# Kernel tuning notes

Measured on AMD Instinct MI355X. Metric: run time of the kernel, lower is better.

## Reference

```python
import jax, jax.numpy as jnp
import numpy as np

EPS = 1e-5

def _conv(x, w, pad):
    # x: [B,C,H,W] NCHW, w: [O,I,kh,kw] OIHW
    return jax.lax.conv_general_dilated(
        x, w, (1, 1), [(pad, pad), (pad, pad)],
        dimension_numbers=('NCHW', 'OIHW', 'NCHW'))

def _bn(x, g, b, m, v):
    # eval-mode batchnorm folded into scale/shift
    s = g * jax.lax.rsqrt(v + EPS)
    return x * s[None, :, None, None] + (b - m * s)[None, :, None, None]

def _cbr(x, w, g, b, m, v):
    # Convolution block from CornerNet: conv3x3(pad=1, no bias) + BN + ReLU
    return jax.nn.relu(_bn(_conv(x, w, 1), g, b, m, v))


def setup_inputs() -> dict:
    key = jax.random.key(0)
    B, Cin, C, H, W = 4, 256, 256, 128, 128
    kdims = {'up': (C, Cin, 3, 3), 'down': (C, Cin, 3, 3),
             'p': (C, C, 3, 3), 'c1': (C, Cin, 1, 1), 'c2': (C, C, 3, 3)}
    inp = {'x': jax.random.normal(key, (B, Cin, H, W), dtype=jnp.float32)}
    for i, n in enumerate(['up', 'down', 'p', 'c1', 'c2']):
        ks = jax.random.split(jax.random.fold_in(key, i + 1), 5)
        inp['w_' + n] = jax.random.normal(ks[0], kdims[n], dtype=jnp.float32) * 0.02
        inp['g_' + n] = 1.0 + 0.1 * jax.random.normal(ks[1], (C,), dtype=jnp.float32)
        inp['b_' + n] = 0.1 * jax.random.normal(ks[2], (C,), dtype=jnp.float32)
        inp['m_' + n] = 0.1 * jax.random.normal(ks[3], (C,), dtype=jnp.float32)
        inp['v_' + n] = 0.5 + jax.random.uniform(ks[4], (C,), dtype=jnp.float32)
    return inp


def reference(x,
              w_up, g_up, b_up, m_up, v_up,
              w_down, g_down, b_down, m_down, v_down,
              w_p, g_p, b_p, m_p, v_p,
              w_c1, g_c1, b_c1, m_c1, v_c1,
              w_c2, g_c2, b_c2, m_c2, v_c2):
    # up branch: conv-bn-relu then LeftPool (reverse cummax over W) then RightPool (cummax over W)
    up = _cbr(x, w_up, g_up, b_up, m_up, v_up)
    up = jax.lax.cummax(up, axis=3, reverse=True)   # LeftPool
    up = jax.lax.cummax(up, axis=3)                 # RightPool
    # down branch: conv-bn-relu then TopPool (reverse cummax over H) then BottomPool (cummax over H)
    down = _cbr(x, w_down, g_down, b_down, m_down, v_down)
    down = jax.lax.cummax(down, axis=2, reverse=True)  # TopPool
    down = jax.lax.cummax(down, axis=2)                # BottomPool
    # merge path: 3x3 conv + BN on pooled sum
    merge = _bn(_conv(up + down, w_p, 1), g_p, b_p, m_p, v_p)
    # shortcut path: 1x1 conv + BN on input
    bn1 = _bn(_conv(x, w_c1, 0), g_c1, b_c1, m_c1, v_c1)
    relu1 = jax.nn.relu(merge + bn1)
    # output Convolution block
    return _cbr(relu1, w_c2, g_c2, b_c2, m_c2, v_c2)
```

## Files before the change

kernel.cpp:

```cpp
#include <hip/hip_runtime.h>

typedef unsigned short u16;
typedef __attribute__((ext_vector_type(8))) short bf16x8;
typedef __attribute__((ext_vector_type(4))) float f32x4;


__device__ __forceinline__ u16 f2bf(float f) {
  unsigned u = __float_as_uint(f);
  unsigned r = u + 0x7fffu + ((u >> 16) & 1u);
  return (u16)(r >> 16);
}

__device__ __forceinline__ void gll16(const char* g, char* l) {
  __builtin_amdgcn_global_load_lds((const __attribute__((address_space(1))) void*)g,
                                   (__attribute__((address_space(3))) void*)l, 16, 0, 0);
}

__global__ void bn_prep_kernel(const float* __restrict__ g, const float* __restrict__ b,
                               const float* __restrict__ m, const float* __restrict__ v,
                               float* __restrict__ st) {
  int c = threadIdx.x;
  float s = g[c] * rsqrtf(v[c] + 1e-5f);
  st[c] = s;
  st[256 + c] = b[c] - m[c] * s;
}

__global__ void bn_fix_kernel(float* __restrict__ st) {
  int c = threadIdx.x;
  st[2 * 512 + 256 + c] += st[3 * 512 + 256 + c];
  st[3 * 512 + c] = st[3 * 512 + c] / st[2 * 512 + c];
}

__global__ void wprep3_kernel(const float* __restrict__ w, u16* __restrict__ dst) {
  int idx = blockIdx.x * 256 + threadIdx.x;
  int blk = idx >> 12, iu = idx & 4095;
  int co_l = iu >> 5, w32 = iu & 31, slot = w32 >> 3, e = w32 & 7;
  int q = slot ^ ((co_l >> 1) & 3);
  int cohalf = blk / 72, step = blk % 72;
  int outer = step / 12, rr = step % 12, dwi = rr >> 2, kc = rr & 3;
  int half = outer / 3, d = outer % 3;
  int s = d * 3 + dwi;
  int ci = half * 128 + kc * 32 + q * 8 + e;
  int co = cohalf * 128 + co_l;
  dst[idx] = f2bf(w[(co * 256 + ci) * 9 + s]);
}

__global__ void wprep1_kernel(const float* __restrict__ w, u16* __restrict__ dst,
                              const float* __restrict__ ratio) {
  int idx = blockIdx.x * 256 + threadIdx.x;
  int blk = idx >> 12, iu = idx & 4095;
  int co_l = iu >> 5, w32 = iu & 31, slot = w32 >> 3, e = w32 & 7;
  int q = slot ^ ((co_l >> 1) & 3);
  int cohalf = blk >> 3, j = blk & 7;
  int half2 = j >> 2, kc = j & 3;
  int ci = half2 * 128 + kc * 32 + q * 8 + e;
  int co = cohalf * 128 + co_l;
  dst[idx] = f2bf(w[co * 256 + ci] * ratio[co]);
}

__global__ __launch_bounds__(256) void nchw_to_nhwc_kernel(const float* __restrict__ x,
                                                           char* __restrict__ xb) {
  __shared__ __align__(16) u16 tl[128 * 130];
  int bh = blockIdx.x; int b = bh >> 7, h = bh & 127;
  int t = threadIdx.x;
  for (int half = 0; half < 2; ++half) {
    __syncthreads();
    for (int i = 0; i < 64; ++i) {
      int cil = i * 2 + (t >> 7);
      int ci = half * 128 + cil;
      int w = t & 127;
      tl[w * 130 + cil] = f2bf(x[(size_t)((b * 256 + ci) * 128 + h) * 128 + w]);
    }
    __syncthreads();
    char* plane = xb + (size_t)(b * 128 + h) * 65536 + half * 32768;
    for (int i = 0; i < 32; ++i) {
      int w = i * 4 + (t >> 6);
      int c2 = (t & 63) * 2;
      unsigned v = *(const unsigned*)&tl[w * 130 + c2];
      *(unsigned*)(plane + w * 256 + ((c2 * 2) ^ (((w + 1) & 7) << 4))) = v;
    }
  }
}

__device__ __forceinline__ void stage_a(const char* wA1, const char* wA2, int step,
                                        char* ldsA0, int buf, int t) {
  const char* src = (step < 72) ? (wA1 + (size_t)step * 8192)
                                : (wA2 + (size_t)(step - 72) * 8192);
  char* dst = ldsA0 + buf * 8192 + t * 16;
  const char* g = src + t * 16;
  gll16(g, dst);
  gll16(g + 4096, dst + 4096);
}

__device__ __forceinline__ void stage_b(const char* plane, char* ldsB, int t) {
  if (plane) {
    char* dst = ldsB + 256 + t * 16;
    const char* g = plane + t * 16;
#pragma unroll
    for (int r = 0; r < 8; ++r) gll16(g + r * 4096, dst + r * 4096);
  } else {
    int4 z = {0, 0, 0, 0};
#pragma unroll
    for (int r = 0; r < 8; ++r) *(int4*)(ldsB + 256 + r * 4096 + t * 16) = z;
  }
}

__device__ __forceinline__ void zero_acc(f32x4 (&acc)[4][4]) {
  f32x4 z = {0.f, 0.f, 0.f, 0.f};
#pragma unroll
  for (int i = 0; i < 4; ++i)
#pragma unroll
    for (int j = 0; j < 4; ++j) acc[i][j] = z;
}

#define CONV_STEP(WP_ADD, KC)                                                              \
  {                                                                                        \
    if (i + 1 < nsteps) {                                                                  \
      stage_a(wA1, wA2, i + 1, ldsA0, cur ^ 1, t);                                         \
      asm volatile("s_waitcnt vmcnt(2) lgkmcnt(0)" ::: "memory");                          \
    } else {                                                                               \
      asm volatile("s_waitcnt vmcnt(0) lgkmcnt(0)" ::: "memory");                          \
    }                                                                                      \
    __builtin_amdgcn_s_barrier();                                                          \
    __builtin_amdgcn_sched_barrier(0);                                                     \
    bf16x8 af[4], bf[4];                                                                   \
    const char* lA = ldsA0 + cur * 8192;                                                   \
    _Pragma("unroll")                                                                      \
    for (int f = 0; f < 4; ++f) af[f] = *(const bf16x8*)(lA + aOff[f]);                    \
    _Pragma("unroll")                                                                      \
    for (int f = 0; f < 4; ++f) {                                                          \
      int wp = wpb[f] + (WP_ADD);                                                          \
      bf[f] = *(const bf16x8*)(ldsB + wp * 256 + (((KC)*64 + q * 16) ^ ((wp & 7) << 4)));  \
    }                                                                                      \
    __builtin_amdgcn_s_setprio(1);                                                         \
    _Pragma("unroll")                                                                      \
    for (int fm = 0; fm < 4; ++fm)                                                         \
      _Pragma("unroll")                                                                    \
      for (int fn = 0; fn < 4; ++fn)                                                       \
        acc[fm][fn] =                                                                      \
            __builtin_amdgcn_mfma_f32_16x16x32_bf16(af[fm], bf[fn], acc[fm][fn], 0, 0, 0); \
    __builtin_amdgcn_s_setprio(0);                                                         \
    __builtin_amdgcn_s_barrier();                                                          \
    cur ^= 1;                                                                              \
    ++i;                                                                                   \
  }

__device__ __forceinline__ void conv_pipeline(const char* inB1, const char* inB2,
                                              const char* wA1, const char* wA2,
                                              int h, int nsteps, char* lds,
                                              f32x4 (&acc)[4][4]) {
  const int t = threadIdx.x;
  const int wv = t >> 6, lane = t & 63;
  const int lane15 = lane & 15, q = lane >> 4;
  const int coq = wv >> 1, wh = wv & 1;
  char* ldsB = lds;
  char* ldsA0 = lds + 33280;

  int aOff[4];
#pragma unroll
  for (int f = 0; f < 4; ++f) {
    int ra = coq * 64 + f * 16 + lane15;
    aOff[f] = ra * 64 + ((q ^ ((ra >> 1) & 3)) << 4);
  }
  int wpb[4];
#pragma unroll
  for (int f = 0; f < 4; ++f) wpb[f] = wh * 64 + f * 16 + lane15;

  {
    int4 z = {0, 0, 0, 0};
    if (t < 16) *(int4*)(ldsB + t * 16) = z;
    else if (t < 32) *(int4*)(ldsB + 33024 + (t - 16) * 16) = z;
  }

  int cur = 0, i = 0;
  for (int outer = 0; outer < 6; ++outer) {
    const int half = (outer >= 3) ? 1 : 0;
    const int d = outer - half * 3;
    const int hs = h + d - 1;
    const char* plane = (hs >= 0 && hs < 128)
                            ? inB1 + (size_t)hs * 65536 + (size_t)half * 32768
                            : nullptr;
    stage_b(plane, ldsB, t);
    if (outer == 0) stage_a(wA1, wA2, 0, ldsA0, 0, t);
#pragma unroll
    for (int dwi = 0; dwi < 3; ++dwi)
#pragma unroll
      for (int kc = 0; kc < 4; ++kc) CONV_STEP(dwi, kc)
  }
  if (nsteps > 72) {
    for (int half2 = 0; half2 < 2; ++half2) {
      stage_b(inB2 + (size_t)h * 65536 + (size_t)half2 * 32768, ldsB, t);
#pragma unroll
      for (int kc = 0; kc < 4; ++kc) CONV_STEP(1, kc)
    }
  }
}

__device__ __forceinline__ void store_pad_relu(f32x4 (&acc)[4][4], const float* __restrict__ st,
                                               int cohalf, int b, int h, char* __restrict__ out) {
  const int t = threadIdx.x, lane = t & 63, wv = t >> 6;
  const int lane15 = lane & 15, q = lane >> 4, coq = wv >> 1, wh = wv & 1;
  char* plane = out + (size_t)(b * 128 + h) * 65536 + cohalf * 32768;
#pragma unroll
  for (int fm = 0; fm < 4; ++fm) {
    int co_l = coq * 64 + fm * 16 + q * 4;
    int co = cohalf * 128 + co_l;
    float ss[4], tt[4];
#pragma unroll
    for (int r = 0; r < 4; ++r) { ss[r] = st[co + r]; tt[r] = st[256 + co + r]; }
#pragma unroll
    for (int fn = 0; fn < 4; ++fn) {
      int w = wh * 64 + fn * 16 + lane15;
      short4 o;
      o.x = (short)f2bf(fmaxf(acc[fm][fn][0] * ss[0] + tt[0], 0.f));
      o.y = (short)f2bf(fmaxf(acc[fm][fn][1] * ss[1] + tt[1], 0.f));
      o.z = (short)f2bf(fmaxf(acc[fm][fn][2] * ss[2] + tt[2], 0.f));
      o.w = (short)f2bf(fmaxf(acc[fm][fn][3] * ss[3] + tt[3], 0.f));
      *(short4*)(plane + w * 256 + ((co_l * 2) ^ (((w + 1) & 7) << 4))) = o;
    }
  }
}

__global__ __launch_bounds__(256, 3) void conv_up_kernel(const char* __restrict__ xb,
                                                         const char* __restrict__ wp,
                                                         const float* __restrict__ st,
                                                         float* __restrict__ rmax) {
  __shared__ __align__(16) char lds[49664];
  int swz = (blockIdx.x & 7) * 64 + (blockIdx.x >> 3);
  int b = swz >> 7, h = swz & 127;
  int cohalf = blockIdx.y;
  const char* wA = wp + (size_t)cohalf * 589824;
  f32x4 acc[4][4];
  zero_acc(acc);
  conv_pipeline(xb + (size_t)b * 8388608, nullptr, wA, wA, h, 72, lds, acc);

  const int t = threadIdx.x, lane = t & 63, wv = t >> 6;
  const int lane15 = lane & 15, q = lane >> 4, coq = wv >> 1, wh = wv & 1;
  float* rlds = (float*)lds;
  __syncthreads();
#pragma unroll
  for (int fm = 0; fm < 4; ++fm) {
    int co_l = coq * 64 + fm * 16 + q * 4;
    int co = cohalf * 128 + co_l;
#pragma unroll
    for (int r = 0; r < 4; ++r) {
      float ss = st[co + r], tt = st[256 + co + r];
      float v = 0.f;
#pragma unroll
      for (int fn = 0; fn < 4; ++fn) v = fmaxf(v, acc[fm][fn][r] * ss + tt);
      v = fmaxf(v, __shfl_xor(v, 1));
      v = fmaxf(v, __shfl_xor(v, 2));
      v = fmaxf(v, __shfl_xor(v, 4));
      v = fmaxf(v, __shfl_xor(v, 8));
      if (lane15 == 0) rlds[wh * 128 + co_l + r] = v;
    }
  }
  __syncthreads();
  if (t < 128)
    rmax[(size_t)(b * 128 + h) * 256 + cohalf * 128 + t] = fmaxf(rlds[t], rlds[128 + t]);
}

__global__ __launch_bounds__(256, 3) void conv_down_kernel(const char* __restrict__ xb,
                                                           const char* __restrict__ wp,
                                                           const float* __restrict__ st,
                                                           char* __restrict__ out) {
  __shared__ __align__(16) char lds[49664];
  int swz = (blockIdx.x & 7) * 64 + (blockIdx.x >> 3);
  int b = swz >> 7, h = swz & 127;
  int cohalf = blockIdx.y;
  const char* wA = wp + (size_t)cohalf * 589824;
  f32x4 acc[4][4];
  zero_acc(acc);
  conv_pipeline(xb + (size_t)b * 8388608, nullptr, wA, wA, h, 72, lds, acc);
  store_pad_relu(acc, st, cohalf, b, h, out);
}

__global__ __launch_bounds__(256) void colmax_kernel(const char* __restrict__ dp,
                                                     float* __restrict__ cmax) {
  int bw = blockIdx.x; int b = bw >> 7, w = bw & 127;
  int c = threadIdx.x;
  size_t base = (size_t)b * 8388608 + (size_t)(c >> 7) * 32768 + w * 256 +
                (((c & 127) * 2) ^ (((w + 1) & 7) << 4));
  float m = 0.f;
  for (int h = 0; h < 128; ++h) {
    u16 raw = *(const u16*)(dp + base + (size_t)h * 65536);
    m = fmaxf(m, __uint_as_float(((unsigned)raw) << 16));
  }
  cmax[(size_t)(b * 128 + w) * 256 + c] = m;
}

__global__ __launch_bounds__(256) void pooled_kernel(const float* __restrict__ rmax,
                                                     const float* __restrict__ cmax,
                                                     char* __restrict__ dp) {
  int bh = blockIdx.x; int b = bh >> 7, h = bh & 127;
  int t = threadIdx.x;
  char* plane = dp + (size_t)(b * 128 + h) * 65536;
  const float* rm = rmax + (size_t)(b * 128 + h) * 256;
#pragma unroll
  for (int it = 0; it < 16; ++it) {
    int id = it * 256 + t;
    int half = id >> 11, rem = id & 2047;
    int w = rem >> 4, slot = rem & 15;
    int c0 = half * 128 + slot * 8;
    const float* cm = cmax + (size_t)(b * 128 + w) * 256 + c0;
    const float* rr = rm + c0;
    u16 e[8];
#pragma unroll
    for (int k = 0; k < 8; ++k) e[k] = f2bf(rr[k] + cm[k]);
    int4 v;
    v.x = (int)(e[0] | ((unsigned)e[1] << 16));
    v.y = (int)(e[2] | ((unsigned)e[3] << 16));
    v.z = (int)(e[4] | ((unsigned)e[5] << 16));
    v.w = (int)(e[6] | ((unsigned)e[7] << 16));
    *(int4*)(plane + half * 32768 + w * 256 + ((slot ^ ((w + 1) & 7)) << 4)) = v;
  }
}

__global__ __launch_bounds__(256, 3) void conv_merge_kernel(const char* __restrict__ dp,
                                                            const char* __restrict__ xb,
                                                            const char* __restrict__ wp_p,
                                                            const char* __restrict__ wp_c1,
                                                            const float* __restrict__ st,
                                                            char* __restrict__ out) {
  __shared__ __align__(16) char lds[49664];
  int swz = (blockIdx.x & 7) * 64 + (blockIdx.x >> 3);
  int b = swz >> 7, h = swz & 127;
  int cohalf = blockIdx.y;
  f32x4 acc[4][4];
  zero_acc(acc);
  conv_pipeline(dp + (size_t)b * 8388608, xb + (size_t)b * 8388608,
                wp_p + (size_t)cohalf * 589824, wp_c1 + (size_t)cohalf * 65536,
                h, 80, lds, acc);
  store_pad_relu(acc, st, cohalf, b, h, out);
}

__global__ __launch_bounds__(256, 3) void conv_c2_kernel(const char* __restrict__ relu1,
                                                         const char* __restrict__ wp,
                                                         const float* __restrict__ st,
                                                         float* __restrict__ out) {
  __shared__ __align__(16) char lds[49664];
  int swz = (blockIdx.x & 7) * 64 + (blockIdx.x >> 3);
  int b = swz >> 7, h = swz & 127;
  int cohalf = blockIdx.y;
  const char* wA = wp + (size_t)cohalf * 589824;
  f32x4 acc[4][4];
  zero_acc(acc);
  conv_pipeline(relu1 + (size_t)b * 8388608, nullptr, wA, wA, h, 72, lds, acc);

  const int t = threadIdx.x, lane = t & 63, wv = t >> 6;
  const int lane15 = lane & 15, q = lane >> 4, coq = wv >> 1, wh = wv & 1;
  float* tl = (float*)lds;
  for (int g = 0; g < 8; ++g) {
    __syncthreads();
    if (coq == (g >> 2)) {
      int fm = g & 3;
      int co_l = coq * 64 + fm * 16 + q * 4;
      int co = cohalf * 128 + co_l;
#pragma unroll
      for (int r = 0; r < 4; ++r) {
        float ss = st[co + r], tt = st[256 + co + r];
#pragma unroll
        for (int fn = 0; fn < 4; ++fn) {
          int w = wh * 64 + fn * 16 + lane15;
          tl[(q * 4 + r) * 132 + w] = fmaxf(acc[fm][fn][r] * ss + tt, 0.f);
        }
      }
    }
    __syncthreads();
    int row = t >> 4, ch = t & 15;
    int co = cohalf * 128 + g * 16 + row;
    float* dst = out + (size_t)((b * 256 + co) * 128 + h) * 128 + ch * 8;
    float4 p0 = *(float4*)&tl[row * 132 + ch * 8];
    float4 p1 = *(float4*)&tl[row * 132 + ch * 8 + 4];
    *(float4*)dst = p0;
    *(float4*)(dst + 4) = p1;
  }
}

extern "C" void kernel_launch(void* const* d_in, const int* in_sizes, int n_in,
                              void* d_out, int out_size, void* d_ws, size_t ws_size,
                              hipStream_t stream) {
  (void)in_sizes; (void)n_in; (void)out_size; (void)ws_size;
  const float* x    = (const float*)d_in[0];
  const float* w_up = (const float*)d_in[1];
  const float* w_dn = (const float*)d_in[6];
  const float* w_p  = (const float*)d_in[11];
  const float* w_c1 = (const float*)d_in[16];
  const float* w_c2 = (const float*)d_in[21];

  char* ws = (char*)d_ws;
  char* xb    = ws;
  char* dp    = ws + 33554432ull;
  char* relu1 = ws + 67108864ull;
  char* wp_up = ws + 100663296ull;
  char* wp_dn = ws + 101842944ull;
  char* wp_p  = ws + 103022592ull;
  char* wp_c2 = ws + 104202240ull;
  char* wp_c1 = ws + 105381888ull;
  float* st   = (float*)(ws + 105512960ull);
  float* rmax = (float*)(ws + 105523200ull);
  float* cmax = (float*)(ws + 106047488ull);

  bn_prep_kernel<<<1, 256, 0, stream>>>((const float*)d_in[2], (const float*)d_in[3],
                                        (const float*)d_in[4], (const float*)d_in[5], st);
  bn_prep_kernel<<<1, 256, 0, stream>>>((const float*)d_in[7], (const float*)d_in[8],
                                        (const float*)d_in[9], (const float*)d_in[10], st + 512);
  bn_prep_kernel<<<1, 256, 0, stream>>>((const float*)d_in[12], (const float*)d_in[13],
                                        (const float*)d_in[14], (const float*)d_in[15], st + 1024);
  bn_prep_kernel<<<1, 256, 0, stream>>>((const float*)d_in[17], (const float*)d_in[18],
                                        (const float*)d_in[19], (const float*)d_in[20], st + 1536);
  bn_prep_kernel<<<1, 256, 0, stream>>>((const float*)d_in[22], (const float*)d_in[23],
                                        (const float*)d_in[24], (const float*)d_in[25], st + 2048);
  bn_fix_kernel<<<1, 256, 0, stream>>>(st);

  wprep3_kernel<<<2304, 256, 0, stream>>>(w_up, (u16*)wp_up);
  wprep3_kernel<<<2304, 256, 0, stream>>>(w_dn, (u16*)wp_dn);
  wprep3_kernel<<<2304, 256, 0, stream>>>(w_p, (u16*)wp_p);
  wprep3_kernel<<<2304, 256, 0, stream>>>(w_c2, (u16*)wp_c2);
  wprep1_kernel<<<256, 256, 0, stream>>>(w_c1, (u16*)wp_c1, st + 1536);

  nchw_to_nhwc_kernel<<<512, 256, 0, stream>>>(x, xb);

  conv_up_kernel<<<dim3(512, 2), 256, 0, stream>>>(xb, wp_up, st, rmax);
  conv_down_kernel<<<dim3(512, 2), 256, 0, stream>>>(xb, wp_dn, st + 512, dp);
  colmax_kernel<<<512, 256, 0, stream>>>(dp, cmax);
  pooled_kernel<<<512, 256, 0, stream>>>(rmax, cmax, dp);
  conv_merge_kernel<<<dim3(512, 2), 256, 0, stream>>>(dp, xb, wp_p, wp_c1, st + 1024, relu1);
  conv_c2_kernel<<<dim3(512, 2), 256, 0, stream>>>(relu1, wp_c2, st + 2048, (float*)d_out);
}
```

Measured before the change: 399.5 us.

## Give each wave a private weight double-buffer to drop per-step block barriers

Each wave now stages its own copy of the weight tile into a private LDS double-buffer, and waits only on its own vmcnt. This removes the two block-wide barriers per K-step; block barriers remain only around the per-plane B staging. Waves that share a cout quarter load the same weights twice, which doubles weight LDS traffic. LDS per block grows from about 49 KB to 66 KB, and launch bounds drop from 3 to 2 blocks per CU, lowering occupancy.

```diff
diff --git a/kernel.cpp b/kernel.cpp
--- a/kernel.cpp
+++ b/kernel.cpp
@@ -82,14 +82,14 @@
   }
 }
 
-__device__ __forceinline__ void stage_a(const char* wA1, const char* wA2, int step,
-                                        char* ldsA0, int buf, int t) {
+__device__ __forceinline__ void stage_aw(const char* wA1, const char* wA2, int step,
+                                         char* ldsAw, int buf, int coq, int lane) {
   const char* src = (step < 72) ? (wA1 + (size_t)step * 8192)
                                 : (wA2 + (size_t)(step - 72) * 8192);
-  char* dst = ldsA0 + buf * 8192 + t * 16;
-  const char* g = src + t * 16;
-  gll16(g, dst);
-  gll16(g + 4096, dst + 4096);
+  const char* g = src + coq * 4096 + lane * 16;
+  char* dst = ldsAw + buf * 4096 + lane * 16;
+#pragma unroll
+  for (int k = 0; k < 4; ++k) gll16(g + k * 1024, dst + k * 1024);
 }
 
 __device__ __forceinline__ void stage_b(const char* plane, char* ldsB, int t) {
@@ -116,15 +116,13 @@
 #define CONV_STEP(WP_ADD, KC)                                                              \
   {                                                                                        \
     if (i + 1 < nsteps) {                                                                  \
-      stage_a(wA1, wA2, i + 1, ldsA0, cur ^ 1, t);                                         \
-      asm volatile("s_waitcnt vmcnt(2) lgkmcnt(0)" ::: "memory");                          \
+      stage_aw(wA1, wA2, i + 1, ldsAw, cur ^ 1, coq, lane);                                \
+      asm volatile("s_waitcnt vmcnt(4)" ::: "memory");                                     \
     } else {                                                                               \
-      asm volatile("s_waitcnt vmcnt(0) lgkmcnt(0)" ::: "memory");                          \
+      asm volatile("s_waitcnt vmcnt(0)" ::: "memory");                                     \
     }                                                                                      \
-    __builtin_amdgcn_s_barrier();                                                          \
-    __builtin_amdgcn_sched_barrier(0);                                                     \
     bf16x8 af[4], bf[4];                                                                   \
-    const char* lA = ldsA0 + cur * 8192;                                                   \
+    const char* lA = ldsAw + cur * 4096;                                                   \
     _Pragma("unroll")                                                                      \
     for (int f = 0; f < 4; ++f) af[f] = *(const bf16x8*)(lA + aOff[f]);                    \
     _Pragma("unroll")                                                                      \
@@ -140,7 +138,6 @@
         acc[fm][fn] =                                                                      \
             __builtin_amdgcn_mfma_f32_16x16x32_bf16(af[fm], bf[fn], acc[fm][fn], 0, 0, 0); \
     __builtin_amdgcn_s_setprio(0);                                                         \
-    __builtin_amdgcn_s_barrier();                                                          \
     cur ^= 1;                                                                              \
     ++i;                                                                                   \
   }
@@ -154,12 +151,12 @@
   const int lane15 = lane & 15, q = lane >> 4;
   const int coq = wv >> 1, wh = wv & 1;
   char* ldsB = lds;
-  char* ldsA0 = lds + 33280;
+  char* ldsAw = lds + 33280 + wv * 8192;
 
   int aOff[4];
 #pragma unroll
   for (int f = 0; f < 4; ++f) {
-    int ra = coq * 64 + f * 16 + lane15;
+    int ra = f * 16 + lane15;
     aOff[f] = ra * 64 + ((q ^ ((ra >> 1) & 3)) << 4);
   }
   int wpb[4];
@@ -171,6 +168,8 @@
     if (t < 16) *(int4*)(ldsB + t * 16) = z;
     else if (t < 32) *(int4*)(ldsB + 33024 + (t - 16) * 16) = z;
   }
+
+  stage_aw(wA1, wA2, 0, ldsAw, 0, coq, lane);
 
   int cur = 0, i = 0;
   for (int outer = 0; outer < 6; ++outer) {
@@ -180,8 +179,11 @@
     const char* plane = (hs >= 0 && hs < 128)
                             ? inB1 + (size_t)hs * 65536 + (size_t)half * 32768
                             : nullptr;
+    asm volatile("s_waitcnt lgkmcnt(0)" ::: "memory");
+    __builtin_amdgcn_s_barrier();
     stage_b(plane, ldsB, t);
-    if (outer == 0) stage_a(wA1, wA2, 0, ldsA0, 0, t);
+    asm volatile("s_waitcnt vmcnt(0) lgkmcnt(0)" ::: "memory");
+    __builtin_amdgcn_s_barrier();
 #pragma unroll
     for (int dwi = 0; dwi < 3; ++dwi)
 #pragma unroll
@@ -189,7 +191,11 @@
   }
   if (nsteps > 72) {
     for (int half2 = 0; half2 < 2; ++half2) {
+      asm volatile("s_waitcnt lgkmcnt(0)" ::: "memory");
+      __builtin_amdgcn_s_barrier();
       stage_b(inB2 + (size_t)h * 65536 + (size_t)half2 * 32768, ldsB, t);
+      asm volatile("s_waitcnt vmcnt(0) lgkmcnt(0)" ::: "memory");
+      __builtin_amdgcn_s_barrier();
 #pragma unroll
       for (int kc = 0; kc < 4; ++kc) CONV_STEP(1, kc)
     }
@@ -221,11 +227,11 @@
   }
 }
 
-__global__ __launch_bounds__(256, 3) void conv_up_kernel(const char* __restrict__ xb,
+__global__ __launch_bounds__(256, 2) void conv_up_kernel(const char* __restrict__ xb,
                                                          const char* __restrict__ wp,
                                                          const float* __restrict__ st,
                                                          float* __restrict__ rmax) {
-  __shared__ __align__(16) char lds[49664];
+  __shared__ __align__(16) char lds[66048];
   int swz = (blockIdx.x & 7) * 64 + (blockIdx.x >> 3);
   int b = swz >> 7, h = swz & 127;
   int cohalf = blockIdx.y;
@@ -260,11 +266,11 @@
     rmax[(size_t)(b * 128 + h) * 256 + cohalf * 128 + t] = fmaxf(rlds[t], rlds[128 + t]);
 }
 
-__global__ __launch_bounds__(256, 3) void conv_down_kernel(const char* __restrict__ xb,
+__global__ __launch_bounds__(256, 2) void conv_down_kernel(const char* __restrict__ xb,
                                                            const char* __restrict__ wp,
                                                            const float* __restrict__ st,
                                                            char* __restrict__ out) {
-  __shared__ __align__(16) char lds[49664];
+  __shared__ __align__(16) char lds[66048];
   int swz = (blockIdx.x & 7) * 64 + (blockIdx.x >> 3);
   int b = swz >> 7, h = swz & 127;
   int cohalf = blockIdx.y;
@@ -316,13 +322,13 @@
   }
 }
 
-__global__ __launch_bounds__(256, 3) void conv_merge_kernel(const char* __restrict__ dp,
+__global__ __launch_bounds__(256, 2) void conv_merge_kernel(const char* __restrict__ dp,
                                                             const char* __restrict__ xb,
                                                             const char* __restrict__ wp_p,
                                                             const char* __restrict__ wp_c1,
                                                             const float* __restrict__ st,
                                                             char* __restrict__ out) {
-  __shared__ __align__(16) char lds[49664];
+  __shared__ __align__(16) char lds[66048];
   int swz = (blockIdx.x & 7) * 64 + (blockIdx.x >> 3);
   int b = swz >> 7, h = swz & 127;
   int cohalf = blockIdx.y;
@@ -334,11 +340,11 @@
   store_pad_relu(acc, st, cohalf, b, h, out);
 }
 
-__global__ __launch_bounds__(256, 3) void conv_c2_kernel(const char* __restrict__ relu1,
+__global__ __launch_bounds__(256, 2) void conv_c2_kernel(const char* __restrict__ relu1,
                                                          const char* __restrict__ wp,
                                                          const float* __restrict__ st,
                                                          float* __restrict__ out) {
-  __shared__ __align__(16) char lds[49664];
+  __shared__ __align__(16) char lds[66048];
   int swz = (blockIdx.x & 7) * 64 + (blockIdx.x >> 3);
   int b = swz >> 7, h = swz & 127;
   int cohalf = blockIdx.y;
```

After: 397.7 us. About the same (-0.5%).
